# Kernel tuning notes

Hardware: AMD Instinct MI355X
Metric: run time of the kernel (lower is better)

## Reference

```python
import jax, jax.numpy as jnp
import numpy as np
import math

EMBED_DIM = 1024
NUM_HEADS = 16
HEAD_DIM = EMBED_DIM // NUM_HEADS
BATCH = 2
SEQ = 2048


def alibi_slopes(num_heads):
    def pow2_slopes(n):
        start = 2.0 ** (-(2.0 ** (-(math.log2(n) - 3))))
        return [start * (start ** i) for i in range(n)]
    if math.log2(num_heads).is_integer():
        s = pow2_slopes(num_heads)
    else:
        closest = 2 ** math.floor(math.log2(num_heads))
        s = pow2_slopes(closest)
        s += s[-1:] * (num_heads - closest)
    return jnp.asarray(s, dtype=jnp.float32)  # [H]


def setup_inputs() -> dict:
    key = jax.random.key(0)
    k1, k2, k3, k4, k5 = jax.random.split(key, 5)
    x = jax.random.normal(k1, (BATCH, SEQ, EMBED_DIM), dtype=jnp.float32)
    sd = 1.0 / math.sqrt(EMBED_DIM)
    Wqkv = jax.random.uniform(k2, (EMBED_DIM, 3 * EMBED_DIM), minval=-sd, maxval=sd, dtype=jnp.float32)
    bqkv = jax.random.uniform(k3, (3 * EMBED_DIM,), minval=-sd, maxval=sd, dtype=jnp.float32)
    Wout = jax.random.uniform(k4, (EMBED_DIM, EMBED_DIM), minval=-sd, maxval=sd, dtype=jnp.float32)
    bout = jax.random.uniform(k5, (EMBED_DIM,), minval=-sd, maxval=sd, dtype=jnp.float32)
    return {"x": x, "Wqkv": Wqkv, "bqkv": bqkv, "Wout": Wout, "bout": bout}


def reference(x, Wqkv, bqkv, Wout, bout):
    B, S, E = x.shape
    H, D = NUM_HEADS, HEAD_DIM
    qkv = x @ Wqkv + bqkv                       # [B,S,3E]
    qkv = qkv.reshape(B, S, H, 3 * D)
    q, k, v = jnp.split(qkv, 3, axis=-1)        # each [B,S,H,D]
    scores = jnp.einsum('bqhd,bkhd->bhqk', q, k) / math.sqrt(D)
    # ALiBi bias: distance[i,j] = j - i, scaled per-head
    pos = jnp.arange(S)
    distance = (pos[None, :] - pos[:, None]).astype(jnp.float32)  # [S,S]
    scores = scores + alibi_slopes(H)[None, :, None, None] * distance[None, None, :, :]
    attn = jax.nn.softmax(scores, axis=-1)      # [B,H,S,S]
    out = jnp.einsum('bhqk,bkhd->bqhd', attn, v).reshape(B, S, E)
    out = out @ Wout + bout
    return out, attn
```

## Files before the change

### kernel.cpp

```cpp
#include <hip/hip_runtime.h>

#define BATCH 2
#define SEQ   2048
#define EMB   1024
#define NH    16
#define HD    64

typedef __attribute__((ext_vector_type(8))) _Float16 half8;
typedef __attribute__((ext_vector_type(4))) _Float16 half4;
typedef __attribute__((ext_vector_type(4))) float floatx4;

#define LOG2E 1.44269504088896f
#define SCALE2 (0.125f * LOG2E)

#if __has_builtin(__builtin_amdgcn_exp2f)
__device__ __forceinline__ float fexp2(float x) { return __builtin_amdgcn_exp2f(x); }
#else
__device__ __forceinline__ float fexp2(float x) { return exp2f(x); }
#endif

__device__ __forceinline__ void lds_barrier() {
    asm volatile("s_waitcnt lgkmcnt(0)" ::: "memory");
    __builtin_amdgcn_s_barrier();
    __builtin_amdgcn_sched_barrier(0);
}

__global__ __launch_bounds__(256)
void cvt_f16(const float* __restrict__ in, _Float16* __restrict__ out, int n8) {
    int i = blockIdx.x * 256 + threadIdx.x;
    if (i >= n8) return;
    float4 a = ((const float4*)in)[2 * i];
    float4 b = ((const float4*)in)[2 * i + 1];
    half8 h = {(_Float16)a.x, (_Float16)a.y, (_Float16)a.z, (_Float16)a.w,
               (_Float16)b.x, (_Float16)b.y, (_Float16)b.z, (_Float16)b.w};
    ((half8*)out)[i] = h;
}

__global__ __launch_bounds__(256)
void transpose_both(const float* __restrict__ Wqkv, const float* __restrict__ Wout,
                    _Float16* __restrict__ Wh, _Float16* __restrict__ Oh) {
    __shared__ float t[32][33];
    const int K = EMB;
    const float* W; _Float16* o; int N, n0;
    if (blockIdx.x < 96) { W = Wqkv; o = Wh; N = 3 * EMB; n0 = blockIdx.x * 32; }
    else                 { W = Wout; o = Oh; N = EMB;     n0 = (blockIdx.x - 96) * 32; }
    const int k0 = blockIdx.y * 32;
    const int r = threadIdx.x >> 3, c4 = (threadIdx.x & 7) * 4;
    float4 v = *(const float4*)&W[(size_t)(k0 + r) * N + n0 + c4];
    t[r][c4 + 0] = v.x; t[r][c4 + 1] = v.y;
    t[r][c4 + 2] = v.z; t[r][c4 + 3] = v.w;
    __syncthreads();
    half4 hv;
#pragma unroll
    for (int j = 0; j < 4; ++j) hv[j] = (_Float16)t[c4 + j][r];
    *(half4*)&o[(size_t)(n0 + r) * K + k0 + c4] = hv;
}

#define ALD 40

__global__ __launch_bounds__(256)
void gemm_qkv_mfma(const _Float16* __restrict__ Xh, const _Float16* __restrict__ Wh,
                   const float* __restrict__ bias,
                   _Float16* __restrict__ Qh, _Float16* __restrict__ Kh,
                   _Float16* __restrict__ Vh) {
    const int K = EMB;
    __shared__ _Float16 Ah[2][128 * ALD];
    __shared__ _Float16 Bh[2][128 * ALD];

    const int tid  = threadIdx.x;
    const int wave = tid >> 6, lane = tid & 63;
    const int quad = lane >> 4, lp = lane & 15;

    const int linear = blockIdx.y * 24 + blockIdx.x;
    const int swz = (linear & 7) * 96 + (linear >> 3);
    const int bx = swz % 24, by = swz / 24;
    const int row0 = by * 128, col0 = bx * 128;
    const int wm = (wave >> 1) * 64, wn = (wave & 1) * 64;

    const int srow = tid >> 2, sseg = (tid & 3) * 8;

    floatx4 acc[4][4];
#pragma unroll
    for (int i = 0; i < 4; ++i)
#pragma unroll
        for (int j = 0; j < 4; ++j) acc[i][j] = (floatx4){0.f, 0.f, 0.f, 0.f};

    uint4 a0 = *(const uint4*)&Xh[(size_t)(row0 + srow) * K + sseg];
    uint4 a1 = *(const uint4*)&Xh[(size_t)(row0 + srow + 64) * K + sseg];
    uint4 b0 = *(const uint4*)&Wh[(size_t)(col0 + srow) * K + sseg];
    uint4 b1 = *(const uint4*)&Wh[(size_t)(col0 + srow + 64) * K + sseg];
    *(uint4*)&Ah[0][srow * ALD + sseg] = a0;
    *(uint4*)&Ah[0][(srow + 64) * ALD + sseg] = a1;
    *(uint4*)&Bh[0][srow * ALD + sseg] = b0;
    *(uint4*)&Bh[0][(srow + 64) * ALD + sseg] = b1;

    int cur = 0;
    for (int k0 = 0; k0 < K; k0 += 32) {
        __syncthreads();
        if (k0 + 32 < K) {
            a0 = *(const uint4*)&Xh[(size_t)(row0 + srow) * K + k0 + 32 + sseg];
            a1 = *(const uint4*)&Xh[(size_t)(row0 + srow + 64) * K + k0 + 32 + sseg];
            b0 = *(const uint4*)&Wh[(size_t)(col0 + srow) * K + k0 + 32 + sseg];
            b1 = *(const uint4*)&Wh[(size_t)(col0 + srow + 64) * K + k0 + 32 + sseg];
        }

        half8 ah[4];
#pragma unroll
        for (int mi = 0; mi < 4; ++mi)
            ah[mi] = *(const half8*)&Ah[cur][(wm + mi * 16 + lp) * ALD + quad * 8];
#pragma unroll
        for (int ni = 0; ni < 4; ++ni) {
            half8 bh = *(const half8*)&Bh[cur][(wn + ni * 16 + lp) * ALD + quad * 8];
#pragma unroll
            for (int mi = 0; mi < 4; ++mi)
                acc[mi][ni] = __builtin_amdgcn_mfma_f32_16x16x32_f16(
                    ah[mi], bh, acc[mi][ni], 0, 0, 0);
        }

        if (k0 + 32 < K) {
            *(uint4*)&Ah[cur ^ 1][srow * ALD + sseg] = a0;
            *(uint4*)&Ah[cur ^ 1][(srow + 64) * ALD + sseg] = a1;
            *(uint4*)&Bh[cur ^ 1][srow * ALD + sseg] = b0;
            *(uint4*)&Bh[cur ^ 1][(srow + 64) * ALD + sseg] = b1;
            cur ^= 1;
        }
    }

#pragma unroll
    for (int ni = 0; ni < 4; ++ni) {
        const int c = col0 + wn + ni * 16 + lp;
        const int h = c / 192;
        const int rem = c - h * 192;
        const int which = rem >> 6;
        const int d = rem & 63;
        _Float16* __restrict__ P = (which == 0) ? Qh : (which == 1) ? Kh : Vh;
        const float bb = bias[c];
        const float sc = (which == 0) ? SCALE2 : 1.0f;
#pragma unroll
        for (int mi = 0; mi < 4; ++mi) {
            floatx4 a = acc[mi][ni];
#pragma unroll
            for (int r = 0; r < 4; ++r) {
                int m = row0 + wm + mi * 16 + quad * 4 + r;
                int b = m >> 11, s = m & (SEQ - 1);
                P[((size_t)(b * NH + h) * SEQ + s) * HD + d] =
                    (_Float16)((a[r] + bb) * sc);
            }
        }
    }
}

__global__ __launch_bounds__(256)
void gemm_out_mfma(const _Float16* __restrict__ Ch, const _Float16* __restrict__ Oh,
                   const float* __restrict__ bias, float* __restrict__ out) {
    const int K = EMB, N = EMB;
    __shared__ _Float16 Ah[2][128 * ALD];
    __shared__ _Float16 Bh[2][128 * ALD];

    const int tid  = threadIdx.x;
    const int wave = tid >> 6, lane = tid & 63;
    const int quad = lane >> 4, lp = lane & 15;

    const int linear = blockIdx.y * 8 + blockIdx.x;
    const int swz = (linear & 7) * 32 + (linear >> 3);
    const int bx = swz & 7, by = swz >> 3;
    const int row0 = by * 128, col0 = bx * 128;
    const int wm = (wave >> 1) * 64, wn = (wave & 1) * 64;

    const int srow = tid >> 2, sseg = (tid & 3) * 8;

    floatx4 acc[4][4];
#pragma unroll
    for (int i = 0; i < 4; ++i)
#pragma unroll
        for (int j = 0; j < 4; ++j) acc[i][j] = (floatx4){0.f, 0.f, 0.f, 0.f};

    uint4 a0 = *(const uint4*)&Ch[(size_t)(row0 + srow) * K + sseg];
    uint4 a1 = *(const uint4*)&Ch[(size_t)(row0 + srow + 64) * K + sseg];
    uint4 b0 = *(const uint4*)&Oh[(size_t)(col0 + srow) * K + sseg];
    uint4 b1 = *(const uint4*)&Oh[(size_t)(col0 + srow + 64) * K + sseg];
    *(uint4*)&Ah[0][srow * ALD + sseg] = a0;
    *(uint4*)&Ah[0][(srow + 64) * ALD + sseg] = a1;
    *(uint4*)&Bh[0][srow * ALD + sseg] = b0;
    *(uint4*)&Bh[0][(srow + 64) * ALD + sseg] = b1;

    int cur = 0;
    for (int k0 = 0; k0 < K; k0 += 32) {
        __syncthreads();
        if (k0 + 32 < K) {
            a0 = *(const uint4*)&Ch[(size_t)(row0 + srow) * K + k0 + 32 + sseg];
            a1 = *(const uint4*)&Ch[(size_t)(row0 + srow + 64) * K + k0 + 32 + sseg];
            b0 = *(const uint4*)&Oh[(size_t)(col0 + srow) * K + k0 + 32 + sseg];
            b1 = *(const uint4*)&Oh[(size_t)(col0 + srow + 64) * K + k0 + 32 + sseg];
        }

        half8 ah[4];
#pragma unroll
        for (int mi = 0; mi < 4; ++mi)
            ah[mi] = *(const half8*)&Ah[cur][(wm + mi * 16 + lp) * ALD + quad * 8];
#pragma unroll
        for (int ni = 0; ni < 4; ++ni) {
            half8 bh = *(const half8*)&Bh[cur][(wn + ni * 16 + lp) * ALD + quad * 8];
#pragma unroll
            for (int mi = 0; mi < 4; ++mi)
                acc[mi][ni] = __builtin_amdgcn_mfma_f32_16x16x32_f16(
                    ah[mi], bh, acc[mi][ni], 0, 0, 0);
        }

        if (k0 + 32 < K) {
            *(uint4*)&Ah[cur ^ 1][srow * ALD + sseg] = a0;
            *(uint4*)&Ah[cur ^ 1][(srow + 64) * ALD + sseg] = a1;
            *(uint4*)&Bh[cur ^ 1][srow * ALD + sseg] = b0;
            *(uint4*)&Bh[cur ^ 1][(srow + 64) * ALD + sseg] = b1;
            cur ^= 1;
        }
    }

#pragma unroll
    for (int ni = 0; ni < 4; ++ni) {
        const int c = col0 + wn + ni * 16 + lp;
        const float bb = bias[c];
#pragma unroll
        for (int mi = 0; mi < 4; ++mi) {
            floatx4 a = acc[mi][ni];
#pragma unroll
            for (int r = 0; r < 4; ++r) {
                int m = row0 + wm + mi * 16 + quad * 4 + r;
                out[(size_t)m * N + c] = a[r] + bb;
            }
        }
    }
}

#define QT 128
#define KT 64
#define LDST 72
#define NTILE (SEQ / KT)

__global__ __launch_bounds__(512)
void attn_mfma(const _Float16* __restrict__ Qh,
               const _Float16* __restrict__ Kh,
               const _Float16* __restrict__ Vh,
               float* __restrict__ attn,
               _Float16* __restrict__ ctx) {
    __shared__ _Float16 ksb[2][KT * LDST];
    __shared__ _Float16 vtb[2][HD * LDST];
    __shared__ _Float16 ps[QT * LDST];

    const int tid  = threadIdx.x;
    const int wave = tid >> 6, lane = tid & 63;
    const int quad = lane >> 4, lp = lane & 15;
    const int q0 = blockIdx.x * QT;
    const int bh = blockIdx.y;
    const int h  = bh & (NH - 1);
    const float slope2 = exp2f(-0.5f * (float)(h + 1)) * LOG2E;

    const _Float16* Qbase = Qh + ((size_t)bh * SEQ + q0) * HD;
    const _Float16* Kbase = Kh + (size_t)bh * SEQ * HD;
    const _Float16* Vbase = Vh + (size_t)bh * SEQ * HD;

    const half8 qa0 = *(const half8*)&Qbase[(size_t)(16 * wave + lp) * HD + quad * 8];
    const half8 qa1 = *(const half8*)&Qbase[(size_t)(16 * wave + lp) * HD + 32 + quad * 8];

    const int qg = q0 + 16 * wave + lp;
    const float aq = -slope2 * (float)qg;

    const int srow = tid >> 3, sseg = tid & 7;
    const int kvx = srow ^ (sseg << 3);

    float m0 = -1e30f, mxv = -1e30f, lsum = 0.f;

    uint4 kreg = *(const uint4*)&Kbase[(size_t)srow * HD + sseg * 8];
    *(uint4*)&ksb[0][srow * LDST + sseg * 8] = kreg;
    lds_barrier();

    int cur = 0;
    for (int kt = 0; kt < NTILE; ++kt) {
        if (kt) lds_barrier();
        if (kt + 1 < NTILE)
            kreg = *(const uint4*)&Kbase[(size_t)(kt + 1) * KT * HD +
                                         (size_t)srow * HD + sseg * 8];
        const _Float16* ks = ksb[cur];

        floatx4 cc[4];
        __builtin_amdgcn_s_setprio(1);
#pragma unroll
        for (int t = 0; t < 4; ++t) {
            half8 b0 = *(const half8*)&ks[(16 * t + lp) * LDST + quad * 8];
            half8 b1 = *(const half8*)&ks[(16 * t + lp) * LDST + 32 + quad * 8];
            floatx4 c = {0.f, 0.f, 0.f, 0.f};
            c = __builtin_amdgcn_mfma_f32_16x16x32_f16(b0, qa0, c, 0, 0, 0);
            cc[t] = __builtin_amdgcn_mfma_f32_16x16x32_f16(b1, qa1, c, 0, 0, 0);
        }
        __builtin_amdgcn_s_setprio(0);
#pragma unroll
        for (int t = 0; t < 4; ++t) {
            float kb = (float)(kt * KT + 16 * t + 4 * quad);
            float s0 = cc[t][0] + fmaf(slope2, kb,       aq);
            float s1 = cc[t][1] + fmaf(slope2, kb + 1.f, aq);
            float s2 = cc[t][2] + fmaf(slope2, kb + 2.f, aq);
            float s3 = cc[t][3] + fmaf(slope2, kb + 3.f, aq);
            float tm = fmaxf(fmaxf(s0, s1), fmaxf(s2, s3));
            mxv = fmaxf(mxv, tm);
            if (mxv > m0 + 8.f) {
                lsum *= fexp2(m0 - mxv);
                m0 = mxv;
            }
            lsum += fexp2(s0 - m0) + fexp2(s1 - m0) +
                    fexp2(s2 - m0) + fexp2(s3 - m0);
        }

        if (kt + 1 < NTILE) {
            *(uint4*)&ksb[cur ^ 1][srow * LDST + sseg * 8] = kreg;
            cur ^= 1;
        }
    }

    float off2;
    {
        float mm = mxv;
        float ll = lsum * fexp2(m0 - mm);
#pragma unroll
        for (int off = 16; off < 64; off <<= 1) {
            float mo = __shfl_xor(mm, off);
            float lo = __shfl_xor(ll, off);
            float mn = fmaxf(mm, mo);
            ll = ll * fexp2(mm - mn) + lo * fexp2(mo - mn);
            mm = mn;
        }
        off2 = mm + __log2f(ll);
    }

    floatx4 o[4];
#pragma unroll
    for (int t = 0; t < 4; ++t) o[t] = (floatx4){0.f, 0.f, 0.f, 0.f};

    float* arow = attn + (size_t)bh * SEQ * SEQ +
                  (size_t)(q0 + 16 * wave + lp) * SEQ + 4 * quad;
    const float aq2 = aq - off2;

    lds_barrier();
    uint4 vreg;
    kreg = *(const uint4*)&Kbase[(size_t)srow * HD + sseg * 8];
    vreg = *(const uint4*)&Vbase[(size_t)srow * HD + sseg * 8];
    *(uint4*)&ksb[0][srow * LDST + sseg * 8] = kreg;
    {
        union { uint4 u; _Float16 e[8]; } vv; vv.u = vreg;
#pragma unroll
        for (int j = 0; j < 8; ++j)
            vtb[0][(sseg * 8 + j) * LDST + kvx] = vv.e[j];
    }
    lds_barrier();

    cur = 0;
    for (int kt = 0; kt < NTILE; ++kt) {
        if (kt) lds_barrier();
        if (kt + 1 < NTILE) {
            size_t goff = (size_t)(kt + 1) * KT * HD + (size_t)srow * HD + sseg * 8;
            kreg = *(const uint4*)&Kbase[goff];
            vreg = *(const uint4*)&Vbase[goff];
        }
        const _Float16* ks = ksb[cur];
        const _Float16* vt = vtb[cur];

        __builtin_amdgcn_s_setprio(1);
#pragma unroll
        for (int t = 0; t < 4; ++t) {
            half8 b0 = *(const half8*)&ks[(16 * t + lp) * LDST + quad * 8];
            half8 b1 = *(const half8*)&ks[(16 * t + lp) * LDST + 32 + quad * 8];
            floatx4 c = {0.f, 0.f, 0.f, 0.f};
            c = __builtin_amdgcn_mfma_f32_16x16x32_f16(b0, qa0, c, 0, 0, 0);
            c = __builtin_amdgcn_mfma_f32_16x16x32_f16(b1, qa1, c, 0, 0, 0);
            float kb = (float)(kt * KT + 16 * t + 4 * quad);
            float p0 = fexp2(c[0] + fmaf(slope2, kb,       aq2));
            float p1 = fexp2(c[1] + fmaf(slope2, kb + 1.f, aq2));
            float p2 = fexp2(c[2] + fmaf(slope2, kb + 2.f, aq2));
            float p3 = fexp2(c[3] + fmaf(slope2, kb + 3.f, aq2));
            float4 pw = {p0, p1, p2, p3};
            *(float4*)&arow[kt * KT + 16 * t] = pw;
            const int col = 16 * t + 4 * quad;
            half4 ph = {(_Float16)p0, (_Float16)p1, (_Float16)p2, (_Float16)p3};
            *(half4*)&ps[(16 * wave + lp) * LDST + col] = ph;
        }
        __builtin_amdgcn_s_setprio(0);

        half8 pa0 = *(const half8*)&ps[(16 * wave + lp) * LDST + quad * 8];
        half8 pa1 = *(const half8*)&ps[(16 * wave + lp) * LDST + 32 + quad * 8];
        __builtin_amdgcn_s_setprio(1);
#pragma unroll
        for (int t = 0; t < 4; ++t) {
            int g = 2 * t + (lp >> 3);
            half8 vb0 = *(const half8*)&vt[(16 * t + lp) * LDST + ((quad ^ g) << 3)];
            half8 vb1 = *(const half8*)&vt[(16 * t + lp) * LDST + (((quad + 4) ^ g) << 3)];
            o[t] = __builtin_amdgcn_mfma_f32_16x16x32_f16(pa0, vb0, o[t], 0, 0, 0);
            o[t] = __builtin_amdgcn_mfma_f32_16x16x32_f16(pa1, vb1, o[t], 0, 0, 0);
        }
        __builtin_amdgcn_s_setprio(0);

        if (kt + 1 < NTILE) {
            *(uint4*)&ksb[cur ^ 1][srow * LDST + sseg * 8] = kreg;
            union { uint4 u; _Float16 e[8]; } vv; vv.u = vreg;
#pragma unroll
            for (int j = 0; j < 8; ++j)
                vtb[cur ^ 1][(sseg * 8 + j) * LDST + kvx] = vv.e[j];
            cur ^= 1;
        }
    }

    const int b = bh >> 4;
#pragma unroll
    for (int t = 0; t < 4; ++t)
#pragma unroll
        for (int r = 0; r < 4; ++r)
            ctx[((size_t)(b * SEQ + q0 + 16 * wave + quad * 4 + r)) * EMB +
                h * HD + 16 * t + lp] = (_Float16)o[t][r];
}


extern "C" void kernel_launch(void* const* d_in, const int* in_sizes, int n_in,
                              void* d_out, int out_size, void* d_ws, size_t ws_size,
                              hipStream_t stream) {
    const float* x    = (const float*)d_in[0];
    const float* Wqkv = (const float*)d_in[1];
    const float* bqkv = (const float*)d_in[2];
    const float* Wout = (const float*)d_in[3];
    const float* bout = (const float*)d_in[4];

    float* out  = (float*)d_out;
    float* attn = out + (size_t)BATCH * SEQ * EMB;

    const size_t HE = (size_t)BATCH * NH * SEQ * HD;
    const size_t XE = (size_t)BATCH * SEQ * EMB;
    _Float16* Qh = (_Float16*)d_ws;
    _Float16* Kh = Qh + HE;
    _Float16* Vh = Kh + HE;
    _Float16* Ch = Vh + HE;
    _Float16* Xh = Ch + XE;
    _Float16* Wh = Xh + XE;
    _Float16* Oh = Wh + (size_t)3 * EMB * EMB;

    cvt_f16<<<dim3(2048), dim3(256), 0, stream>>>(x, Xh, (int)(XE / 8));
    transpose_both<<<dim3(128, 32), dim3(256), 0, stream>>>(Wqkv, Wout, Wh, Oh);

    gemm_qkv_mfma<<<dim3(24, 32), dim3(256), 0, stream>>>(
        Xh, Wh, bqkv, Qh, Kh, Vh);

    attn_mfma<<<dim3(SEQ / QT, BATCH * NH), dim3(512), 0, stream>>>(
        Qh, Kh, Vh, attn, Ch);

    gemm_out_mfma<<<dim3(8, 32), dim3(256), 0, stream>>>(Ch, Oh, bout, out);
}
```

Before: 257.3 us.

## Split attention into separate softmax-stats kernel and PV/attn-write kernel

The fused two-pass attention kernel is split into two launches. attn_stats computes per-row log-sum-exp offsets with 64-query blocks of 256 threads and writes them to a workspace buffer. attn_pv then reloads those offsets and does the probability write-out and PV product. The aim is more blocks and better occupancy for the stats pass, and lighter, separately scheduled kernels. The cost is an extra launch, a small global round-trip, and K being streamed once more.

New measurement: 258.7 us. No clear change (+0.5%).

```diff
diff --git a/kernel.cpp b/kernel.cpp
--- a/kernel.cpp
+++ b/kernel.cpp
@@ -232,32 +232,26 @@
     }
 }
 
-#define QT 128
 #define KT 64
 #define LDST 72
 #define NTILE (SEQ / KT)
 
-__global__ __launch_bounds__(512)
-void attn_mfma(const _Float16* __restrict__ Qh,
-               const _Float16* __restrict__ Kh,
-               const _Float16* __restrict__ Vh,
-               float* __restrict__ attn,
-               _Float16* __restrict__ ctx) {
+__global__ __launch_bounds__(256)
+void attn_stats(const _Float16* __restrict__ Qh,
+                const _Float16* __restrict__ Kh,
+                float* __restrict__ off2g) {
     __shared__ _Float16 ksb[2][KT * LDST];
-    __shared__ _Float16 vtb[2][HD * LDST];
-    __shared__ _Float16 ps[QT * LDST];
 
     const int tid  = threadIdx.x;
     const int wave = tid >> 6, lane = tid & 63;
     const int quad = lane >> 4, lp = lane & 15;
-    const int q0 = blockIdx.x * QT;
+    const int q0 = blockIdx.x * 64;
     const int bh = blockIdx.y;
     const int h  = bh & (NH - 1);
     const float slope2 = exp2f(-0.5f * (float)(h + 1)) * LOG2E;
 
     const _Float16* Qbase = Qh + ((size_t)bh * SEQ + q0) * HD;
     const _Float16* Kbase = Kh + (size_t)bh * SEQ * HD;
-    const _Float16* Vbase = Vh + (size_t)bh * SEQ * HD;
 
     const half8 qa0 = *(const half8*)&Qbase[(size_t)(16 * wave + lp) * HD + quad * 8];
     const half8 qa1 = *(const half8*)&Qbase[(size_t)(16 * wave + lp) * HD + 32 + quad * 8];
@@ -265,21 +259,24 @@
     const int qg = q0 + 16 * wave + lp;
     const float aq = -slope2 * (float)qg;
 
-    const int srow = tid >> 3, sseg = tid & 7;
-    const int kvx = srow ^ (sseg << 3);
+    const int srow0 = tid >> 3, srow1 = 32 + (tid >> 3), sseg = tid & 7;
 
     float m0 = -1e30f, mxv = -1e30f, lsum = 0.f;
 
-    uint4 kreg = *(const uint4*)&Kbase[(size_t)srow * HD + sseg * 8];
-    *(uint4*)&ksb[0][srow * LDST + sseg * 8] = kreg;
+    uint4 k0r = *(const uint4*)&Kbase[(size_t)srow0 * HD + sseg * 8];
+    uint4 k1r = *(const uint4*)&Kbase[(size_t)srow1 * HD + sseg * 8];
+    *(uint4*)&ksb[0][srow0 * LDST + sseg * 8] = k0r;
+    *(uint4*)&ksb[0][srow1 * LDST + sseg * 8] = k1r;
     lds_barrier();
 
     int cur = 0;
     for (int kt = 0; kt < NTILE; ++kt) {
         if (kt) lds_barrier();
-        if (kt + 1 < NTILE)
-            kreg = *(const uint4*)&Kbase[(size_t)(kt + 1) * KT * HD +
-                                         (size_t)srow * HD + sseg * 8];
+        if (kt + 1 < NTILE) {
+            size_t goff = (size_t)(kt + 1) * KT * HD + sseg * 8;
+            k0r = *(const uint4*)&Kbase[goff + (size_t)srow0 * HD];
+            k1r = *(const uint4*)&Kbase[goff + (size_t)srow1 * HD];
+        }
         const _Float16* ks = ksb[cur];
 
         floatx4 cc[4];
@@ -311,25 +308,60 @@
         }
 
         if (kt + 1 < NTILE) {
-            *(uint4*)&ksb[cur ^ 1][srow * LDST + sseg * 8] = kreg;
+            *(uint4*)&ksb[cur ^ 1][srow0 * LDST + sseg * 8] = k0r;
+            *(uint4*)&ksb[cur ^ 1][srow1 * LDST + sseg * 8] = k1r;
             cur ^= 1;
         }
     }
 
-    float off2;
-    {
-        float mm = mxv;
-        float ll = lsum * fexp2(m0 - mm);
-#pragma unroll
-        for (int off = 16; off < 64; off <<= 1) {
-            float mo = __shfl_xor(mm, off);
-            float lo = __shfl_xor(ll, off);
-            float mn = fmaxf(mm, mo);
-            ll = ll * fexp2(mm - mn) + lo * fexp2(mo - mn);
-            mm = mn;
-        }
-        off2 = mm + __log2f(ll);
-    }
+    float mm = mxv;
+    float ll = lsum * fexp2(m0 - mm);
+#pragma unroll
+    for (int off = 16; off < 64; off <<= 1) {
+        float mo = __shfl_xor(mm, off);
+        float lo = __shfl_xor(ll, off);
+        float mn = fmaxf(mm, mo);
+        ll = ll * fexp2(mm - mn) + lo * fexp2(mo - mn);
+        mm = mn;
+    }
+    if (quad == 0)
+        off2g[(size_t)bh * SEQ + qg] = mm + __log2f(ll);
+}
+
+#define QT 128
+
+__global__ __launch_bounds__(512)
+void attn_pv(const _Float16* __restrict__ Qh,
+             const _Float16* __restrict__ Kh,
+             const _Float16* __restrict__ Vh,
+             const float* __restrict__ off2g,
+             float* __restrict__ attn,
+             _Float16* __restrict__ ctx) {
+    __shared__ _Float16 ksb[2][KT * LDST];
+    __shared__ _Float16 vtb[2][HD * LDST];
+    __shared__ _Float16 ps[QT * LDST];
+
+    const int tid  = threadIdx.x;
+    const int wave = tid >> 6, lane = tid & 63;
+    const int quad = lane >> 4, lp = lane & 15;
+    const int q0 = blockIdx.x * QT;
+    const int bh = blockIdx.y;
+    const int h  = bh & (NH - 1);
+    const float slope2 = exp2f(-0.5f * (float)(h + 1)) * LOG2E;
+
+    const _Float16* Qbase = Qh + ((size_t)bh * SEQ + q0) * HD;
+    const _Float16* Kbase = Kh + (size_t)bh * SEQ * HD;
+    const _Float16* Vbase = Vh + (size_t)bh * SEQ * HD;
+
+    const half8 qa0 = *(const half8*)&Qbase[(size_t)(16 * wave + lp) * HD + quad * 8];
+    const half8 qa1 = *(const half8*)&Qbase[(size_t)(16 * wave + lp) * HD + 32 + quad * 8];
+
+    const int qg = q0 + 16 * wave + lp;
+    const float off2 = off2g[(size_t)bh * SEQ + qg];
+    const float aq2 = -slope2 * (float)qg - off2;
+
+    const int srow = tid >> 3, sseg = tid & 7;
+    const int kvx = srow ^ (sseg << 3);
 
     floatx4 o[4];
 #pragma unroll
@@ -337,10 +369,8 @@
 
     float* arow = attn + (size_t)bh * SEQ * SEQ +
                   (size_t)(q0 + 16 * wave + lp) * SEQ + 4 * quad;
-    const float aq2 = aq - off2;
-
-    lds_barrier();
-    uint4 vreg;
+
+    uint4 kreg, vreg;
     kreg = *(const uint4*)&Kbase[(size_t)srow * HD + sseg * 8];
     vreg = *(const uint4*)&Vbase[(size_t)srow * HD + sseg * 8];
     *(uint4*)&ksb[0][srow * LDST + sseg * 8] = kreg;
@@ -352,7 +382,7 @@
     }
     lds_barrier();
 
-    cur = 0;
+    int cur = 0;
     for (int kt = 0; kt < NTILE; ++kt) {
         if (kt) lds_barrier();
         if (kt + 1 < NTILE) {
@@ -438,6 +468,7 @@
     _Float16* Xh = Ch + XE;
     _Float16* Wh = Xh + XE;
     _Float16* Oh = Wh + (size_t)3 * EMB * EMB;
+    float* off2g = (float*)(Oh + (size_t)EMB * EMB);
 
     cvt_f16<<<dim3(2048), dim3(256), 0, stream>>>(x, Xh, (int)(XE / 8));
     transpose_both<<<dim3(128, 32), dim3(256), 0, stream>>>(Wqkv, Wout, Wh, Oh);
@@ -445,8 +476,11 @@
     gemm_qkv_mfma<<<dim3(24, 32), dim3(256), 0, stream>>>(
         Xh, Wh, bqkv, Qh, Kh, Vh);
 
-    attn_mfma<<<dim3(SEQ / QT, BATCH * NH), dim3(512), 0, stream>>>(
-        Qh, Kh, Vh, attn, Ch);
+    attn_stats<<<dim3(SEQ / 64, BATCH * NH), dim3(256), 0, stream>>>(
+        Qh, Kh, off2g);
+
+    attn_pv<<<dim3(SEQ / QT, BATCH * NH), dim3(512), 0, stream>>>(
+        Qh, Kh, Vh, off2g, attn, Ch);
 
     gemm_out_mfma<<<dim3(8, 32), dim3(256), 0, stream>>>(Ch, Oh, bout, out);
 }
```
